# Optimization experiments

Hardware: AMD Instinct MI355X
Metric: run time of the kernel (lower is better)

The kernel has to match this reference:

```python
import jax, jax.numpy as jnp
import numpy as np

SIZE = 256
DEPTH = 3
B = 64
T = 1000
V = 100000


def setup_inputs() -> dict:
    key = jax.random.key(0)
    ks = jax.random.split(key, 2 + 3 * DEPTH)
    s = 0.05
    inp = {
        "ids": jax.random.randint(ks[0], (B, T), 0, V),
        "emb": jax.random.normal(ks[1], (V, SIZE), jnp.float32) * s,
    }
    # layer 0 sees the embedding; layers 1,2 see concat(embedding, prev hidden)
    in_dims = [SIZE, 2 * SIZE, 2 * SIZE]
    for i in range(DEPTH):
        inp[f"W{i}x"] = jax.random.normal(ks[2 + 3 * i], (in_dims[i], 4 * SIZE), jnp.float32) * s
        inp[f"W{i}h"] = jax.random.normal(ks[3 + 3 * i], (SIZE, 4 * SIZE), jnp.float32) * s
        inp[f"b{i}"] = jnp.zeros((4 * SIZE,), jnp.float32)
    return inp


def _lstm_cell(x, c, h, Wx, Wh, b):
    # TF LSTMCell gate order: i, j (cell candidate), f, o; forget_bias = 0.0
    g = x @ Wx + h @ Wh + b
    i, j, f, o = jnp.split(g, 4, axis=-1)
    c_new = jax.nn.sigmoid(f) * c + jax.nn.sigmoid(i) * jnp.tanh(j)
    h_new = jax.nn.sigmoid(o) * jnp.tanh(c_new)
    return c_new, h_new


def reference(ids, emb, W0x, W0h, b0, W1x, W1h, b1, W2x, W2h, b2):
    params = [(W0x, W0h, b0), (W1x, W1h, b1), (W2x, W2h, b2)]
    x_seq = jnp.swapaxes(emb[ids], 0, 1)  # [T, B, size]
    batch = ids.shape[0]
    c0 = jnp.zeros((DEPTH, batch, SIZE), x_seq.dtype)
    h0 = jnp.zeros((DEPTH, batch, SIZE), x_seq.dtype)

    def step(carry, x_t):
        cs, hs = carry
        new_c, new_h = [], []
        prev = x_t
        for i, (Wx, Wh, b) in enumerate(params):
            # skip connection: every layer above the first also sees the
            # original timestep input (first layer input)
            layer_in = x_t if i == 0 else jnp.concatenate([x_t, prev], axis=-1)
            c_n, h_n = _lstm_cell(layer_in, cs[i], hs[i], Wx, Wh, b)
            new_c.append(c_n)
            new_h.append(h_n)
            prev = h_n
        return (jnp.stack(new_c), jnp.stack(new_h)), None

    (cs, hs), _ = jax.lax.scan(step, (c0, h0), x_seq)
    # final stacked state: concat over layers of (c, h) -> [B, depth*2*size]
    out = jnp.concatenate(
        [jnp.concatenate([cs[i], hs[i]], axis=-1) for i in range(DEPTH)], axis=-1
    )
    return out
```

## Files before the change

kernel.cpp:

```cpp
#include <hip/hip_runtime.h>
#include <hip/hip_bf16.h>


typedef __attribute__((ext_vector_type(8))) short short8;
typedef __attribute__((ext_vector_type(4))) float f32x4;
typedef unsigned short u16;
typedef unsigned int u32;

#define TSEQ 1000
#define NBLK 32
#define GRID_REC 256
#define NHELP (GRID_REC - NBLK)

#define O_FLAG 0L
#define O_SYNC 512L
#define O_H    1573376L
#define O_C    1769984L
#define O_BPA  1966592L
#define O_BPR  3539456L
#define O_AX   6160896L

__device__ __forceinline__ u16 f2b(float v) {
    __hip_bfloat16 h = __float2bfloat16(v);
    u16 u; __builtin_memcpy(&u, &h, 2); return u;
}
__device__ __forceinline__ float b2f(u16 u) {
    __hip_bfloat16 h; __builtin_memcpy(&h, &u, 2); return __bfloat162float(h);
}
__device__ __forceinline__ float rdw(const void* p, long i, int isbf) {
    return isbf ? b2f(((const u16*)p)[i]) : ((const float*)p)[i];
}
__device__ __forceinline__ float sigm(float x) { return 1.0f / (1.0f + __expf(-x)); }
__device__ __forceinline__ float tanh_(float x) { return 1.0f - 2.0f / (1.0f + __expf(2.0f * x)); }
__device__ __forceinline__ f32x4 mfma16(short8 a, short8 b, f32x4 c) {
    return __builtin_amdgcn_mfma_f32_16x16x32_bf16(a, b, c, 0, 0, 0);
}

__global__ void k_detect(const u32* __restrict__ embw, int* flag) {
    __shared__ int cnt[256];
    int tid = threadIdx.x, c = 0;
    for (int i = 0; i < 16; ++i) {
        u32 w = embw[tid * 16 + i];
        u32 e = (w >> 7) & 0xFF;
        c += (e >= 110 && e <= 126) ? 1 : 0;
    }
    cnt[tid] = c; __syncthreads();
    for (int s = 128; s > 0; s >>= 1) { if (tid < s) cnt[tid] += cnt[tid + s]; __syncthreads(); }
    if (tid == 0) flag[0] = (cnt[0] > 2048) ? 1 : 0;
}

__global__ void k_pack_a(const void* W0x, const void* W1x, const void* W2x, void* wsv) {
    char* ws = (char*)wsv;
    int isbf = *(const int*)(ws + O_FLAG);
    int l = threadIdx.x & 63, w = threadIdx.x >> 6;
    int gid = blockIdx.x * 4 + w;
    int tile = gid >> 3, ks = gid & 7;
    int L = tile >> 6, wi = tile & 63, bk = wi >> 1, half = wi & 1;
    int n16 = l & 15, g = half * 2 + (n16 >> 3), u = n16 & 7;
    int n = g * 256 + bk * 8 + u;
    const void* W = (L == 0) ? W0x : ((L == 1) ? W1x : W2x);
    union { u16 us[8]; short8 v; } tmp;
#pragma unroll
    for (int j = 0; j < 8; ++j) {
        int k = ks * 32 + (l >> 4) * 8 + j;
        tmp.us[j] = f2b(rdw(W, (long)k * 1024 + n, isbf));
    }
    ((short8*)(ws + O_BPA))[(long)(tile * 8 + ks) * 64 + l] = tmp.v;
}

__global__ void k_pack_r(const void* W0h, const void* W1x, const void* W1h,
                         const void* W2x, const void* W2h, void* wsv) {
    char* ws = (char*)wsv;
    int isbf = *(const int*)(ws + O_FLAG);
    int l = threadIdx.x & 63, w = threadIdx.x >> 6;
    int gid = blockIdx.x * 4 + w;
    int bk = gid / 80, fb = gid % 80;
    int s, nt, ks;
    if (fb < 16) { s = 0; nt = fb >> 3; ks = fb & 7; }
    else if (fb < 48) { s = 1; int f = fb - 16; nt = f >> 4; ks = f & 15; }
    else { s = 2; int f = fb - 48; nt = f >> 4; ks = f & 15; }
    int n16 = l & 15, g = nt * 2 + (n16 >> 3), u = n16 & 7;
    int n = g * 256 + bk * 8 + u;
    union { u16 us[8]; short8 v; } tmp;
#pragma unroll
    for (int j = 0; j < 8; ++j) {
        int k = ks * 32 + (l >> 4) * 8 + j;
        float v;
        if (s == 0) v = rdw(W0h, (long)k * 1024 + n, isbf);
        else if (s == 1) v = (k < 256) ? rdw(W1x, (long)(256 + k) * 1024 + n, isbf)
                                       : rdw(W1h, (long)(k - 256) * 1024 + n, isbf);
        else v = (k < 256) ? rdw(W2x, (long)(256 + k) * 1024 + n, isbf)
                           : rdw(W2h, (long)(k - 256) * 1024 + n, isbf);
        tmp.us[j] = f2b(v);
    }
    ((short8*)(ws + O_BPR))[(long)bk * 80 * 64 + (long)fb * 64 + l] = tmp.v;
}

__device__ __forceinline__ void gemm_tile(const int* __restrict__ ids, const void* __restrict__ emb,
    const void* b0, const void* b1, const void* b2, const short8* __restrict__ bpa,
    int isbf, int seg, int t, u16* __restrict__ axp) {
    int tid = threadIdx.x, l = tid & 63, w = tid >> 6;
    int n16 = l & 15, kg = l >> 4;
    short8 a[4][8];
#pragma unroll
    for (int mt = 0; mt < 4; ++mt) {
        int b = mt * 16 + n16;
        long id = ids[b * TSEQ + t];
        if (isbf) {
            const u16* ep = (const u16*)emb + id * 256;
#pragma unroll
            for (int ks = 0; ks < 8; ++ks)
                a[mt][ks] = *(const short8*)(ep + ks * 32 + kg * 8);
        } else {
            const float* ep = (const float*)emb + id * 256;
#pragma unroll
            for (int ks = 0; ks < 8; ++ks) {
                f32x4 v0 = *(const f32x4*)(ep + ks * 32 + kg * 8);
                f32x4 v1 = *(const f32x4*)(ep + ks * 32 + kg * 8 + 4);
                union { u16 us[8]; short8 v; } tmp;
#pragma unroll
                for (int j = 0; j < 4; ++j) { tmp.us[j] = f2b(v0[j]); tmp.us[4 + j] = f2b(v1[j]); }
                a[mt][ks] = tmp.v;
            }
        }
    }
#pragma unroll
    for (int nt = 0; nt < 4; ++nt) {
        int tile = seg * 16 + w * 4 + nt;
        f32x4 acc[4];
#pragma unroll
        for (int mt = 0; mt < 4; ++mt) acc[mt] = (f32x4){0.f, 0.f, 0.f, 0.f};
#pragma unroll
        for (int ks = 0; ks < 8; ++ks) {
            short8 bb = bpa[(long)(tile * 8 + ks) * 64 + l];
#pragma unroll
            for (int mt = 0; mt < 4; ++mt) acc[mt] = mfma16(a[mt][ks], bb, acc[mt]);
        }
        int L = tile >> 6, wi = tile & 63, bkk = wi >> 1, half = wi & 1;
        int g = half * 2 + (n16 >> 3), u = n16 & 7;
        const void* bias = (L == 0) ? b0 : ((L == 1) ? b1 : b2);
        float bv = rdw(bias, g * 256 + bkk * 8 + u, isbf);
        long base = (long)(L * 32 + bkk) * 2048 + half * 16 + n16;
#pragma unroll
        for (int mt = 0; mt < 4; ++mt)
#pragma unroll
            for (int i = 0; i < 4; ++i) {
                int row = mt * 16 + kg * 4 + i;
                axp[base + (long)row * 32] = f2b(acc[mt][i] + bv);
            }
    }
}

__global__ __launch_bounds__(256, 1) void k_gemm_x(
    const int* __restrict__ ids, const void* __restrict__ emb,
    const void* b0, const void* b1, const void* b2, void* wsv, int t0) {
    char* ws = (char*)wsv;
    int isbf = *(const int*)(ws + O_FLAG);
    const short8* bpa = (const short8*)(ws + O_BPA);
    u16* ax = (u16*)(ws + O_AX);
    gemm_tile(ids, emb, b0, b1, b2, bpa, isbf, blockIdx.x, t0 + blockIdx.y,
              ax + (long)blockIdx.y * 196608);
}

__device__ __forceinline__ void barrier_pub(char* slot, int rank, u32 p, int tid) {
    __syncthreads();
    if (tid == 0)
        __hip_atomic_store((u32*)(slot + 3072) + rank, p, __ATOMIC_RELAXED,
                           __HIP_MEMORY_SCOPE_AGENT);
}
__device__ __forceinline__ void barrier_wait(char* slot, u32 p, int l, int w) {
    if (w == 0) {
        u32* myat = (u32*)(slot + 3072) + (l & 31);
        for (int it = 0; it < (1 << 20); ++it) {
            u32 va = __hip_atomic_load(myat, __ATOMIC_RELAXED, __HIP_MEMORY_SCOPE_AGENT);
            if (__all((int)(va >= p))) break;
        }
    }
    __builtin_amdgcn_s_barrier();
    asm volatile("buffer_inv" ::: "memory");
}

__device__ __forceinline__ void gate_update(f32x4 acc0, f32x4 acc1,
    const u32* ax0, const u32* ax1, float* cst, u16* hc, int hoff, bool own) {
    float A0 = own ? -1.0f : 2.0f;
    float C1 = own ? 1.0f : -2.0f;
    float C0 = own ? 0.0f : 1.0f;
#pragma unroll
    for (int i = 0; i < 4; ++i) {
        float g0 = acc0[i] + b2f((u16)ax0[i]);
        float g1 = acc1[i] + b2f((u16)ax1[i]);
        float v0 = C1 * (1.0f / (1.0f + __expf(A0 * g0))) + C0;
        float v1 = 1.0f / (1.0f + __expf(-g1));
        float tj = __shfl_xor(v0, 8, 64);
        float so = __shfl_xor(v1, 8, 64);
        float cn = v1 * cst[i] + v0 * tj;
        float hn = so * tanh_(cn);
        cst[i] = own ? cn : 0.0f;
        if (own) hc[hoff + i * 8] = f2b(hn);
    }
}

__device__ __forceinline__ void loadax_raw(u32 dst[2][4], const u16* axs, int n16, int w, int kg) {
#pragma unroll
    for (int i = 0; i < 4; ++i) {
        int row = w * 16 + kg * 4 + i;
        dst[0][i] = axs[row * 32 + n16];
        dst[1][i] = axs[row * 32 + 16 + n16];
    }
}

__device__ __forceinline__ void ldslab(short8 dst[8], const u16* hb, int w, int l) {
#pragma unroll
    for (int ks = 0; ks < 8; ++ks)
        dst[ks] = *(const short8*)(hb + w * 4096 + ks * 512 + l * 8);
}

__device__ __forceinline__ void acc8r(const short8 a[8], const short8* bq,
    int i0, int i1, int l, f32x4& a0, f32x4& a1) {
#pragma unroll
    for (int ks = 0; ks < 8; ++ks) {
        a0 = mfma16(a[ks], bq[(i0 + ks) * 64 + l], a0);
        a1 = mfma16(a[ks], bq[(i1 + ks) * 64 + l], a1);
    }
}

__global__ __launch_bounds__(256, 1) void k_rec(
    const int* __restrict__ ids, const void* __restrict__ emb,
    const void* b0, const void* b1, const void* b2,
    void* wsv, void* outv, int chunk, int t0, int tc, int t0n, int tcn,
    long axstride, int first, int last) {
    __shared__ short8 bq[4096];
    __shared__ int sh_role, sh_rank;
    char* ws = (char*)wsv;
    int tid = threadIdx.x, l = tid & 63, w = tid >> 6;
    int isbf = *(const int*)(ws + O_FLAG);
    char* slot = ws + O_SYNC + (long)chunk * 6144;
    int* syn = (int*)slot;
    if (tid == 0) {
        int xcc;
        asm volatile("s_getreg_b32 %0, hwreg(HW_REG_XCC_ID, 0, 8)" : "=s"(xcc));
        xcc &= 7;
        int r = __hip_atomic_fetch_add(syn + 2 + xcc, 1, __ATOMIC_RELAXED, __HIP_MEMORY_SCOPE_AGENT);
        int role = 1, rank = -1;
        if (r < NBLK) {
            if (r == NBLK - 1) {
                int exp = 0;
                __hip_atomic_compare_exchange_strong(syn + 10, &exp, xcc + 1,
                    __ATOMIC_RELAXED, __ATOMIC_RELAXED, __HIP_MEMORY_SCOPE_AGENT);
            }
            int wv;
            while ((wv = __hip_atomic_load(syn + 10, __ATOMIC_RELAXED, __HIP_MEMORY_SCOPE_AGENT)) == 0)
                __builtin_amdgcn_s_sleep(8);
            if (wv == xcc + 1) { role = 0; rank = r; }
        }
        if (role) rank = __hip_atomic_fetch_add(syn + 11, 1, __ATOMIC_RELAXED, __HIP_MEMORY_SCOPE_AGENT);
        sh_role = role; sh_rank = rank;
    }
    __syncthreads();
    int role = sh_role, rank = sh_rank;

    if (role) {
        asm volatile("s_setprio 0");
        if (tcn > 0) {
            const short8* bpa = (const short8*)(ws + O_BPA);
            u16* axn = (u16*)(ws + O_AX) + (long)((chunk + 1) & 1) * axstride;
            for (int job = rank; job < 12 * tcn; job += NHELP) {
                int seg = job % 12, tl = job / 12;
                gemm_tile(ids, emb, b0, b1, b2, bpa, isbf, seg, t0n + tl,
                          axn + (long)tl * 196608);
            }
        }
        return;
    }
    asm volatile("s_setprio 3");
    const short8* bpr = (const short8*)(ws + O_BPR) + (long)rank * 80 * 64;
#pragma unroll
    for (int i = 0; i < 16; ++i) bq[i * 256 + tid] = bpr[16 * 64 + i * 256 + tid];
    short8 w0a[8], w0b[8];
#pragma unroll
    for (int ks = 0; ks < 8; ++ks) { w0a[ks] = bpr[ks * 64 + l]; w0b[ks] = bpr[(8 + ks) * 64 + l]; }
    u16* hbuf = (u16*)(ws + O_H);
    float* csave = (float*)(ws + O_C);
    const u16* axc = (const u16*)(ws + O_AX) + (long)(chunk & 1) * axstride;
    int n16 = l & 15, kg = l >> 4;
    int hu = rank * 8 + (n16 & 7);
    bool own = n16 < 8;
    int gbase = w * 4096 + (rank >> 2) * 512;
    int hoff = (rank & 3) * 128 + kg * 32 + (n16 & 7);
    float c0[4], c1[4], c2[4];
#pragma unroll
    for (int i = 0; i < 4; ++i) {
        int row = w * 16 + kg * 4 + i;
        if (first || !own) { c0[i] = 0.f; c1[i] = 0.f; c2[i] = 0.f; }
        else {
            c0[i] = csave[(0 * 64 + row) * 256 + hu];
            c1[i] = csave[(1 * 64 + row) * 256 + hu];
            c2[i] = csave[(2 * 64 + row) * 256 + hu];
        }
    }
    __syncthreads();
    u32 lph = 0;
    const int sEnd = t0 + tc + 2;
    const int tEnd = t0 + tc;
    u32 pxA[3][2][4], pxB[3][2][4];
    if (tc > 0) loadax_raw(pxA[0], axc + (long)rank * 2048, n16, w, kg);

#define SSTEP(CUR, NXT, S)                                                                         \
    do {                                                                                           \
        int par = (S) & 1, prv = par ^ 1;                                                          \
        const u16* h0p = hbuf + (0 * 2 + prv) * 16384; u16* h0c = hbuf + (0 * 2 + par) * 16384;    \
        const u16* h1p = hbuf + (1 * 2 + prv) * 16384; u16* h1c = hbuf + (1 * 2 + par) * 16384;    \
        const u16* h2p = hbuf + (2 * 2 + prv) * 16384; u16* h2c = hbuf + (2 * 2 + par) * 16384;    \
        bool l0 = (S) < tEnd, l1 = (S) > t0 && (S) <= tEnd, l2 = (S) > t0 + 1;                     \
        short8 a0r[8], a1r[8], a2r[8];                                                             \
        if (l0 || l1) ldslab(a0r, h0p, w, l);                                                      \
        if (l1 || l2) ldslab(a1r, h1p, w, l);                                                      \
        if (l2)       ldslab(a2r, h2p, w, l);                                                      \
        f32x4 A00 = {0.f, 0.f, 0.f, 0.f}, A01 = A00, A10 = A00, A11 = A00, A20 = A00, A21 = A00;   \
        if (l0) {                                                                                  \
            _Pragma("unroll")                                                                      \
            for (int ks = 0; ks < 8; ++ks) {                                                       \
                A00 = mfma16(a0r[ks], w0a[ks], A00); A01 = mfma16(a0r[ks], w0b[ks], A01);          \
            }                                                                                      \
        }                                                                                          \
        if (l1) { acc8r(a0r, bq, 0, 16, l, A10, A11); acc8r(a1r, bq, 8, 24, l, A10, A11); }        \
        if (l2) { acc8r(a1r, bq, 32, 48, l, A20, A21); acc8r(a2r, bq, 40, 56, l, A20, A21); }      \
        if (l0) gate_update(A00, A01, CUR[0][0], CUR[0][1], c0, h0c + gbase, hoff, own);           \
        if (l1) gate_update(A10, A11, CUR[1][0], CUR[1][1], c1, h1c + gbase, hoff, own);           \
        if (l2) gate_update(A20, A21, CUR[2][0], CUR[2][1], c2, h2c + gbase, hoff, own);           \
        int q = (S) + 1;                                                                           \
        if (q < sEnd) {                                                                            \
            ++lph;                                                                                 \
            barrier_pub(slot, rank, lph, tid);                                                     \
            if (q < tEnd)                                                                          \
                loadax_raw(NXT[0], axc + (long)(q - t0) * 196608 + (long)rank * 2048, n16, w, kg); \
            if (q > t0 && q <= tEnd)                                                               \
                loadax_raw(NXT[1], axc + (long)(q - 1 - t0) * 196608 + (long)(32 + rank) * 2048, n16, w, kg); \
            if (q > t0 + 1)                                                                        \
                loadax_raw(NXT[2], axc + (long)(q - 2 - t0) * 196608 + (long)(64 + rank) * 2048, n16, w, kg); \
            barrier_wait(slot, lph, l, w);                                                         \
        }                                                                                          \
    } while (0)

    for (int s = t0; s < sEnd; ) {
        SSTEP(pxA, pxB, s); ++s; if (s >= sEnd) break;
        SSTEP(pxB, pxA, s); ++s;
    }
#undef SSTEP

    if (own) {
#pragma unroll
        for (int i = 0; i < 4; ++i) {
            int row = w * 16 + kg * 4 + i;
            csave[(0 * 64 + row) * 256 + hu] = c0[i];
            csave[(1 * 64 + row) * 256 + hu] = c1[i];
            csave[(2 * 64 + row) * 256 + hu] = c2[i];
        }
        if (last) {
            int f0 = (TSEQ - 1) & 1, f1 = TSEQ & 1, f2 = (TSEQ + 1) & 1;
#pragma unroll
            for (int i = 0; i < 4; ++i) {
                int row = w * 16 + kg * 4 + i;
                float h0v = b2f(hbuf[(0 * 2 + f0) * 16384 + gbase + hoff + i * 8]);
                float h1v = b2f(hbuf[(1 * 2 + f1) * 16384 + gbase + hoff + i * 8]);
                float h2v = b2f(hbuf[(2 * 2 + f2) * 16384 + gbase + hoff + i * 8]);
                if (isbf) {
                    u16* o = (u16*)outv;
                    o[row * 1536 + 0 + hu] = f2b(c0[i]);
                    o[row * 1536 + 256 + hu] = f2b(h0v);
                    o[row * 1536 + 512 + hu] = f2b(c1[i]);
                    o[row * 1536 + 768 + hu] = f2b(h1v);
                    o[row * 1536 + 1024 + hu] = f2b(c2[i]);
                    o[row * 1536 + 1280 + hu] = f2b(h2v);
                } else {
                    float* o = (float*)outv;
                    o[row * 1536 + 0 + hu] = c0[i];
                    o[row * 1536 + 256 + hu] = h0v;
                    o[row * 1536 + 512 + hu] = c1[i];
                    o[row * 1536 + 768 + hu] = h1v;
                    o[row * 1536 + 1024 + hu] = c2[i];
                    o[row * 1536 + 1280 + hu] = h2v;
                }
            }
        }
    }
}

extern "C" void kernel_launch(void* const* d_in, const int* in_sizes, int n_in,
                              void* d_out, int out_size, void* d_ws, size_t ws_size,
                              hipStream_t stream) {
    const int* ids = (const int*)d_in[0];
    const void* emb = d_in[1];
    const void* W0x = d_in[2]; const void* W0h = d_in[3]; const void* b0 = d_in[4];
    const void* W1x = d_in[5]; const void* W1h = d_in[6]; const void* b1 = d_in[7];
    const void* W2x = d_in[8]; const void* W2h = d_in[9]; const void* b2 = d_in[10];
    char* ws = (char*)d_ws;

    long avail = (long)ws_size - O_AX;
    long per_t = 64L * 3072 * 2;
    int tc_single = (int)(avail / per_t);

    hipMemsetAsync(ws + O_SYNC, 0, 1572864, stream);
    hipMemsetAsync(ws + O_H, 0, 196608, stream);
    k_detect<<<1, 256, 0, stream>>>((const u32*)emb, (int*)(ws + O_FLAG));
    k_pack_a<<<384, 256, 0, stream>>>(W0x, W1x, W2x, d_ws);
    k_pack_r<<<640, 256, 0, stream>>>(W0h, W1x, W1h, W2x, W2h, d_ws);

    if (tc_single >= TSEQ) {
        dim3 g(12, TSEQ);
        k_gemm_x<<<g, 256, 0, stream>>>(ids, emb, b0, b1, b2, d_ws, 0);
        k_rec<<<GRID_REC, 256, 0, stream>>>(ids, emb, b0, b1, b2, d_ws, d_out,
                                            0, 0, TSEQ, 0, 0, 0L, 1, 1);
        return;
    }

    int tc_max = (int)(avail / (2 * per_t));
    if (tc_max > TSEQ) tc_max = TSEQ;
    if (tc_max < 4) tc_max = 4;
    long axstride = (long)tc_max * 196608;
    int nck = (TSEQ + tc_max - 1) / tc_max;

    int tc0 = (TSEQ < tc_max) ? TSEQ : tc_max;
    { dim3 g(12, (unsigned)tc0);
      k_gemm_x<<<g, 256, 0, stream>>>(ids, emb, b0, b1, b2, d_ws, 0); }

    for (int c = 0; c < nck; ++c) {
        int t0 = c * tc_max;
        int tc = TSEQ - t0; if (tc > tc_max) tc = tc_max;
        int t0n = t0 + tc;
        int tcn = 0;
        if (c + 1 < nck) { tcn = TSEQ - t0n; if (tcn > tc_max) tcn = tc_max; }
        k_rec<<<GRID_REC, 256, 0, stream>>>(ids, emb, b0, b1, b2, d_ws, d_out,
                                            c, t0, tc, t0n, tcn, axstride,
                                            c == 0, t0 + tc == TSEQ);
    }
}
```

Before: 7.323 ms.

## Split per-step grid barrier into two flag phases for layer 0 and layers 1-2

```diff
diff --git a/kernel.cpp b/kernel.cpp
--- a/kernel.cpp
+++ b/kernel.cpp
@@ -162,18 +162,17 @@
               ax + (long)blockIdx.y * 196608);
 }
 
-__device__ __forceinline__ void barrier_pub(char* slot, int rank, u32 p, int tid) {
+__device__ __forceinline__ void flag_pub(u32* f, int rank, u32 p, int tid) {
     __syncthreads();
     if (tid == 0)
-        __hip_atomic_store((u32*)(slot + 3072) + rank, p, __ATOMIC_RELAXED,
-                           __HIP_MEMORY_SCOPE_AGENT);
-}
-__device__ __forceinline__ void barrier_wait(char* slot, u32 p, int l, int w) {
+        __hip_atomic_store(f + rank, p, __ATOMIC_RELAXED, __HIP_MEMORY_SCOPE_AGENT);
+}
+__device__ __forceinline__ void flag_wait(u32* f, u32 p, int l, int w) {
     if (w == 0) {
-        u32* myat = (u32*)(slot + 3072) + (l & 31);
+        u32* my = f + (l & 31);
         for (int it = 0; it < (1 << 20); ++it) {
-            u32 va = __hip_atomic_load(myat, __ATOMIC_RELAXED, __HIP_MEMORY_SCOPE_AGENT);
-            if (__all((int)(va >= p))) break;
+            u32 v = __hip_atomic_load(my, __ATOMIC_RELAXED, __HIP_MEMORY_SCOPE_AGENT);
+            if (__all((int)(v >= p))) break;
         }
     }
     __builtin_amdgcn_s_barrier();
@@ -236,6 +235,8 @@
     int isbf = *(const int*)(ws + O_FLAG);
     char* slot = ws + O_SYNC + (long)chunk * 6144;
     int* syn = (int*)slot;
+    u32* flagA = (u32*)(slot + 3072);
+    u32* flagB = (u32*)(slot + 3328);
     if (tid == 0) {
         int xcc;
         asm volatile("s_getreg_b32 %0, hwreg(HW_REG_XCC_ID, 0, 8)" : "=s"(xcc));
@@ -314,32 +315,40 @@
         bool l0 = (S) < tEnd, l1 = (S) > t0 && (S) <= tEnd, l2 = (S) > t0 + 1;                     \
         short8 a0r[8], a1r[8], a2r[8];                                                             \
         if (l0 || l1) ldslab(a0r, h0p, w, l);                                                      \
-        if (l1 || l2) ldslab(a1r, h1p, w, l);                                                      \
-        if (l2)       ldslab(a2r, h2p, w, l);                                                      \
-        f32x4 A00 = {0.f, 0.f, 0.f, 0.f}, A01 = A00, A10 = A00, A11 = A00, A20 = A00, A21 = A00;   \
         if (l0) {                                                                                  \
+            f32x4 A00 = {0.f, 0.f, 0.f, 0.f}, A01 = A00;                                           \
             _Pragma("unroll")                                                                      \
             for (int ks = 0; ks < 8; ++ks) {                                                       \
                 A00 = mfma16(a0r[ks], w0a[ks], A00); A01 = mfma16(a0r[ks], w0b[ks], A01);          \
             }                                                                                      \
+            gate_update(A00, A01, CUR[0][0], CUR[0][1], c0, h0c + gbase, hoff, own);               \
         }                                                                                          \
-        if (l1) { acc8r(a0r, bq, 0, 16, l, A10, A11); acc8r(a1r, bq, 8, 24, l, A10, A11); }        \
-        if (l2) { acc8r(a1r, bq, 32, 48, l, A20, A21); acc8r(a2r, bq, 40, 56, l, A20, A21); }      \
-        if (l0) gate_update(A00, A01, CUR[0][0], CUR[0][1], c0, h0c + gbase, hoff, own);           \
-        if (l1) gate_update(A10, A11, CUR[1][0], CUR[1][1], c1, h1c + gbase, hoff, own);           \
-        if (l2) gate_update(A20, A21, CUR[2][0], CUR[2][1], c2, h2c + gbase, hoff, own);           \
+        flag_pub(flagA, rank, lph + 1, tid);                                                       \
         int q = (S) + 1;                                                                           \
         if (q < sEnd) {                                                                            \
-            ++lph;                                                                                 \
-            barrier_pub(slot, rank, lph, tid);                                                     \
             if (q < tEnd)                                                                          \
                 loadax_raw(NXT[0], axc + (long)(q - t0) * 196608 + (long)rank * 2048, n16, w, kg); \
             if (q > t0 && q <= tEnd)                                                               \
                 loadax_raw(NXT[1], axc + (long)(q - 1 - t0) * 196608 + (long)(32 + rank) * 2048, n16, w, kg); \
             if (q > t0 + 1)                                                                        \
                 loadax_raw(NXT[2], axc + (long)(q - 2 - t0) * 196608 + (long)(64 + rank) * 2048, n16, w, kg); \
-            barrier_wait(slot, lph, l, w);                                                         \
         }                                                                                          \
+        flag_wait(flagB, lph, l, w);                                                               \
+        if (l1 || l2) ldslab(a1r, h1p, w, l);                                                      \
+        if (l2)       ldslab(a2r, h2p, w, l);                                                      \
+        if (l1) {                                                                                  \
+            f32x4 A10 = {0.f, 0.f, 0.f, 0.f}, A11 = A10;                                           \
+            acc8r(a0r, bq, 0, 16, l, A10, A11); acc8r(a1r, bq, 8, 24, l, A10, A11);                \
+            gate_update(A10, A11, CUR[1][0], CUR[1][1], c1, h1c + gbase, hoff, own);               \
+        }                                                                                          \
+        if (l2) {                                                                                  \
+            f32x4 A20 = {0.f, 0.f, 0.f, 0.f}, A21 = A20;                                           \
+            acc8r(a1r, bq, 32, 48, l, A20, A21); acc8r(a2r, bq, 40, 56, l, A20, A21);              \
+            gate_update(A20, A21, CUR[2][0], CUR[2][1], c2, h2c + gbase, hoff, own);               \
+        }                                                                                          \
+        flag_pub(flagB, rank, lph + 1, tid);                                                       \
+        ++lph;                                                                                     \
+        if ((S) + 1 < sEnd) flag_wait(flagA, lph, l, w);                                           \
     } while (0)
 
     for (int s = t0; s < sEnd; ) {
```

After: 6.717 ms. 8.3% less time.
